# Kernel tuning notes

Measured on AMD Instinct MI355X. Metric: run time of the kernel, lower is better.

## Reference

```python
import jax, jax.numpy as jnp
import numpy as np
from jax import lax

# LeNet C3 sparse connectivity table: output map -> list of input channels
CONN = [
    [0, 1, 2], [1, 2, 3], [2, 3, 4], [3, 4, 5], [0, 4, 5], [0, 1, 5],          # 6 three-input maps
    [0, 1, 2, 3], [1, 2, 3, 4], [2, 3, 4, 5], [0, 3, 4, 5], [0, 1, 4, 5],      # 9 four-input maps
    [0, 1, 2, 5], [0, 1, 3, 4], [1, 2, 4, 5], [0, 2, 3, 5],
    [0, 1, 2, 3, 4, 5],                                                         # 1 six-input map
]

def _conn_mask():
    m = np.zeros((16, 6), dtype=np.float32)
    for o, chs in enumerate(CONN):
        m[o, chs] = 1.0
    return m[:, :, None, None]  # [O, I, 1, 1]


def setup_inputs() -> dict:
    key = jax.random.key(0)
    kx, kw, kb = jax.random.split(key, 3)
    x = jax.random.normal(kx, (2048, 6, 64, 64), dtype=jnp.float32)
    # fan-in-ish init; only masked entries ever contribute
    W = jax.random.normal(kw, (16, 6, 5, 5), dtype=jnp.float32) * 0.1
    b = jax.random.normal(kb, (16,), dtype=jnp.float32) * 0.01
    return {"x": x, "W": W, "b": b}


def reference(x, W, b):
    # The 16 tiny channel-gathered convs are mathematically a single dense
    # 6->16 VALID 5x5 conv whose weights are zero on non-connected channels.
    Wm = W * jnp.asarray(_conn_mask())                     # [16, 6, 5, 5]
    out = lax.conv_general_dilated(
        x, Wm, window_strides=(1, 1), padding="VALID",
        dimension_numbers=("NCHW", "OIHW", "NCHW"),
    )                                                      # [B, 16, 60, 60]
    return out + b[None, :, None, None]
```

## Files before the change

kernel.cpp:

```cpp
#include <hip/hip_runtime.h>

#define THREADS 384
#define RB 12
#define IN_ROWS 16
#define PS 64
#define LDS_FLOATS (6 * IN_ROWS * PS)

#define DECL(OC) float A0_##OC = bias[OC], A1_##OC = bias[OC]

#define LOADX(IC) do { \
    const float* p_ = brow + (IC) * (IN_ROWS * PS); \
    xa0 = p_[0];      xa1 = p_[1];      xa2 = p_[2];      xa3 = p_[3];      xa4 = p_[4]; \
    xb0 = p_[PS + 0]; xb1 = p_[PS + 1]; xb2 = p_[PS + 2]; xb3 = p_[PS + 3]; xb4 = p_[PS + 4]; \
} while (0)

#define UPD2(OC, IC) do { \
    const float* wp_ = Wky + (OC) * 150 + (IC) * 25; \
    const float w0_ = wp_[0], w1_ = wp_[1], w2_ = wp_[2], w3_ = wp_[3], w4_ = wp_[4]; \
    A0_##OC = fmaf(xa0, w0_, A0_##OC);  A1_##OC = fmaf(xb0, w0_, A1_##OC); \
    A0_##OC = fmaf(xa1, w1_, A0_##OC);  A1_##OC = fmaf(xb1, w1_, A1_##OC); \
    A0_##OC = fmaf(xa2, w2_, A0_##OC);  A1_##OC = fmaf(xb2, w2_, A1_##OC); \
    A0_##OC = fmaf(xa3, w3_, A0_##OC);  A1_##OC = fmaf(xb3, w3_, A1_##OC); \
    A0_##OC = fmaf(xa4, w4_, A0_##OC);  A1_##OC = fmaf(xb4, w4_, A1_##OC); \
} while (0)

#define SBAR __builtin_amdgcn_sched_barrier(0x4 | 0x10 | 0x20 | 0x80 | 0x100)

#define CHAN0 LOADX(0); UPD2(0,0);  UPD2(4,0);  UPD2(5,0);  UPD2(6,0);  UPD2(9,0);  UPD2(10,0); UPD2(11,0); UPD2(12,0); UPD2(14,0); UPD2(15,0); SBAR
#define CHAN1 LOADX(1); UPD2(0,1);  UPD2(1,1);  UPD2(5,1);  UPD2(6,1);  UPD2(7,1);  UPD2(10,1); UPD2(11,1); UPD2(12,1); UPD2(13,1); UPD2(15,1); SBAR
#define CHAN2 LOADX(2); UPD2(0,2);  UPD2(1,2);  UPD2(2,2);  UPD2(6,2);  UPD2(7,2);  UPD2(8,2);  UPD2(11,2); UPD2(13,2); UPD2(14,2); UPD2(15,2); SBAR
#define CHAN3 LOADX(3); UPD2(1,3);  UPD2(2,3);  UPD2(3,3);  UPD2(6,3);  UPD2(7,3);  UPD2(8,3);  UPD2(9,3);  UPD2(12,3); UPD2(14,3); UPD2(15,3); SBAR
#define CHAN4 LOADX(4); UPD2(2,4);  UPD2(3,4);  UPD2(4,4);  UPD2(7,4);  UPD2(8,4);  UPD2(9,4);  UPD2(10,4); UPD2(12,4); UPD2(13,4); UPD2(15,4); SBAR
#define CHAN5 LOADX(5); UPD2(3,5);  UPD2(4,5);  UPD2(5,5);  UPD2(8,5);  UPD2(9,5);  UPD2(10,5); UPD2(11,5); UPD2(13,5); UPD2(14,5); UPD2(15,5); SBAR

#define ST(T, OC) op[(OC) * 3600 + (T) * 60] = A##T##_##OC

__global__ __launch_bounds__(THREADS, 4)
void c3_conv(const float* __restrict__ x, const float* __restrict__ W,
             const float* __restrict__ bias, float* __restrict__ out) {
    __shared__ float xs[LDS_FLOATS + 4];

    const int blk  = blockIdx.x;
    const int img  = blk / 5;
    const int band = blk - img * 5;
    const int r0   = band * RB;
    const int t    = threadIdx.x;

    {
        const float4* src = reinterpret_cast<const float4*>(x) + (size_t)img * 6144;
        float4* dst = reinterpret_cast<float4*>(xs);
        #pragma unroll
        for (int k = 0; k < 4; ++k) {
            int s  = t + k * THREADS;
            int ic = s >> 8;
            int iy = (s >> 4) & 15;
            int c4 = s & 15;
            dst[s] = src[ic * 1024 + (r0 + iy) * 16 + c4];
        }
    }
    __syncthreads();

    const int w    = t >> 6;
    const int lr0  = 2 * w;
    const int lane = t & 63;

    DECL(0);  DECL(1);  DECL(2);  DECL(3);  DECL(4);  DECL(5);  DECL(6);  DECL(7);
    DECL(8);  DECL(9);  DECL(10); DECL(11); DECL(12); DECL(13); DECL(14); DECL(15);

    float xa0, xa1, xa2, xa3, xa4;
    float xb0, xb1, xb2, xb3, xb4;

    #pragma unroll 1
    for (int ky = 0; ky < 5; ++ky) {
        const float* brow = xs + (lr0 + ky) * PS + lane;
        const float* Wky  = W + ky * 5;
        CHAN0; CHAN1; CHAN2; CHAN3; CHAN4; CHAN5;
    }

    if (lane < 60) {
        float* op = out + (size_t)img * 57600 + (size_t)(r0 + lr0) * 60 + lane;
        ST(0,0);  ST(0,1);  ST(0,2);  ST(0,3);  ST(0,4);  ST(0,5);  ST(0,6);  ST(0,7);
        ST(0,8);  ST(0,9);  ST(0,10); ST(0,11); ST(0,12); ST(0,13); ST(0,14); ST(0,15);
        ST(1,0);  ST(1,1);  ST(1,2);  ST(1,3);  ST(1,4);  ST(1,5);  ST(1,6);  ST(1,7);
        ST(1,8);  ST(1,9);  ST(1,10); ST(1,11); ST(1,12); ST(1,13); ST(1,14); ST(1,15);
    }
}

extern "C" void kernel_launch(void* const* d_in, const int* in_sizes, int n_in,
                              void* d_out, int out_size, void* d_ws, size_t ws_size,
                              hipStream_t stream) {
    const float* x  = (const float*)d_in[0];
    const float* W  = (const float*)d_in[1];
    const float* b  = (const float*)d_in[2];
    float* out      = (float*)d_out;

    const int nimg = in_sizes[0] / (6 * 64 * 64);
    dim3 grid(nimg * 5), block(THREADS);
    hipLaunchKernelGGL(c3_conv, grid, block, 0, stream, x, W, b, out);
}
```

Baseline: 319.7 us.

## Drop LDS staging and read input rows directly from global memory

```diff
diff --git a/kernel.cpp b/kernel.cpp
--- a/kernel.cpp
+++ b/kernel.cpp
@@ -1,17 +1,17 @@
 #include <hip/hip_runtime.h>
 
-#define THREADS 384
-#define RB 12
-#define IN_ROWS 16
-#define PS 64
-#define LDS_FLOATS (6 * IN_ROWS * PS)
+#define THREADS 320
+
+typedef float f4 __attribute__((ext_vector_type(4), aligned(4)));
 
 #define DECL(OC) float A0_##OC = bias[OC], A1_##OC = bias[OC]
 
 #define LOADX(IC) do { \
-    const float* p_ = brow + (IC) * (IN_ROWS * PS); \
-    xa0 = p_[0];      xa1 = p_[1];      xa2 = p_[2];      xa3 = p_[3];      xa4 = p_[4]; \
-    xb0 = p_[PS + 0]; xb1 = p_[PS + 1]; xb2 = p_[PS + 2]; xb3 = p_[PS + 3]; xb4 = p_[PS + 4]; \
+    const float* pa_ = xg + (IC) * 4096; \
+    f4 va_ = *(const f4*)pa_;         float a4_ = pa_[4]; \
+    f4 vb_ = *(const f4*)(pa_ + 64);  float b4_ = pa_[68]; \
+    xa0 = va_.x; xa1 = va_.y; xa2 = va_.z; xa3 = va_.w; xa4 = a4_; \
+    xb0 = vb_.x; xb1 = vb_.y; xb2 = vb_.z; xb3 = vb_.w; xb4 = b4_; \
 } while (0)
 
 #define UPD2(OC, IC) do { \
@@ -24,7 +24,7 @@
     A0_##OC = fmaf(xa4, w4_, A0_##OC);  A1_##OC = fmaf(xb4, w4_, A1_##OC); \
 } while (0)
 
-#define SBAR __builtin_amdgcn_sched_barrier(0x4 | 0x10 | 0x20 | 0x80 | 0x100)
+#define SBAR __builtin_amdgcn_sched_barrier(0x4 | 0x10 | 0x20)
 
 #define CHAN0 LOADX(0); UPD2(0,0);  UPD2(4,0);  UPD2(5,0);  UPD2(6,0);  UPD2(9,0);  UPD2(10,0); UPD2(11,0); UPD2(12,0); UPD2(14,0); UPD2(15,0); SBAR
 #define CHAN1 LOADX(1); UPD2(0,1);  UPD2(1,1);  UPD2(5,1);  UPD2(6,1);  UPD2(7,1);  UPD2(10,1); UPD2(11,1); UPD2(12,1); UPD2(13,1); UPD2(15,1); SBAR
@@ -38,31 +38,18 @@
 __global__ __launch_bounds__(THREADS, 4)
 void c3_conv(const float* __restrict__ x, const float* __restrict__ W,
              const float* __restrict__ bias, float* __restrict__ out) {
-    __shared__ float xs[LDS_FLOATS + 4];
+    const int blk  = blockIdx.x;
+    const int img  = blk / 6;
+    const int band = blk - img * 6;
+    const int t    = threadIdx.x;
+    const int w    = t >> 6;
+    const int lane = t & 63;
 
-    const int blk  = blockIdx.x;
-    const int img  = blk / 5;
-    const int band = blk - img * 5;
-    const int r0   = band * RB;
-    const int t    = threadIdx.x;
+    const int pair = band * 5 + w;
+    const int y    = 2 * pair;
+    const int c    = lane < 59 ? lane : 59;
 
-    {
-        const float4* src = reinterpret_cast<const float4*>(x) + (size_t)img * 6144;
-        float4* dst = reinterpret_cast<float4*>(xs);
-        #pragma unroll
-        for (int k = 0; k < 4; ++k) {
-            int s  = t + k * THREADS;
-            int ic = s >> 8;
-            int iy = (s >> 4) & 15;
-            int c4 = s & 15;
-            dst[s] = src[ic * 1024 + (r0 + iy) * 16 + c4];
-        }
-    }
-    __syncthreads();
-
-    const int w    = t >> 6;
-    const int lr0  = 2 * w;
-    const int lane = t & 63;
+    const float* xbase = x + (size_t)img * 24576 + y * 64 + c;
 
     DECL(0);  DECL(1);  DECL(2);  DECL(3);  DECL(4);  DECL(5);  DECL(6);  DECL(7);
     DECL(8);  DECL(9);  DECL(10); DECL(11); DECL(12); DECL(13); DECL(14); DECL(15);
@@ -72,13 +59,13 @@
 
     #pragma unroll 1
     for (int ky = 0; ky < 5; ++ky) {
-        const float* brow = xs + (lr0 + ky) * PS + lane;
-        const float* Wky  = W + ky * 5;
+        const float* xg  = xbase + ky * 64;
+        const float* Wky = W + ky * 5;
         CHAN0; CHAN1; CHAN2; CHAN3; CHAN4; CHAN5;
     }
 
     if (lane < 60) {
-        float* op = out + (size_t)img * 57600 + (size_t)(r0 + lr0) * 60 + lane;
+        float* op = out + (size_t)img * 57600 + (size_t)y * 60 + lane;
         ST(0,0);  ST(0,1);  ST(0,2);  ST(0,3);  ST(0,4);  ST(0,5);  ST(0,6);  ST(0,7);
         ST(0,8);  ST(0,9);  ST(0,10); ST(0,11); ST(0,12); ST(0,13); ST(0,14); ST(0,15);
         ST(1,0);  ST(1,1);  ST(1,2);  ST(1,3);  ST(1,4);  ST(1,5);  ST(1,6);  ST(1,7);
@@ -95,6 +82,6 @@
     float* out      = (float*)d_out;
 
     const int nimg = in_sizes[0] / (6 * 64 * 64);
-    dim3 grid(nimg * 5), block(THREADS);
+    dim3 grid(nimg * 6), block(THREADS);
     hipLaunchKernelGGL(c3_conv, grid, block, 0, stream, x, W, b, out);
 }
```

New measurement: 478.8 us. 49.8% more time.
